# Kernel tuning notes

Hardware: AMD Instinct MI355X
Metric: run time of the kernel (lower is better)

The kernel has to match this reference:

```python
import jax, jax.numpy as jnp
import numpy as np

EPS = 1e-5

def layer_norm(x, g, b):
    mu = jnp.mean(x, axis=-1, keepdims=True)
    var = jnp.var(x, axis=-1, keepdims=True)
    return (x - mu) * jax.lax.rsqrt(var + EPS) * g + b

def setup_inputs() -> dict:
    key = jax.random.key(0)
    ks = jax.random.split(key, 8)
    B, N, C, H = 4, 1024, 1024, 16
    Dh = C * 4
    std = 0.02
    return {
        "x": jax.random.normal(ks[0], (B, N, C), dtype=jnp.float32),
        "qkv_w": jax.random.normal(ks[1], (3 * C, C), dtype=jnp.float32) * std,
        "proj_w": jax.random.normal(ks[2], (C, C), dtype=jnp.float32) * std,
        "proj_b": jnp.zeros((C,), dtype=jnp.float32),
        "fc1_w": jax.random.normal(ks[3], (Dh, C), dtype=jnp.float32) * std,
        "fc1_b": jnp.zeros((Dh,), dtype=jnp.float32),
        "fc2_w": jax.random.normal(ks[4], (C, Dh), dtype=jnp.float32) * std,
        "fc2_b": jnp.zeros((C,), dtype=jnp.float32),
        "ln1_g": jnp.ones((C,), dtype=jnp.float32),
        "ln1_b": jnp.zeros((C,), dtype=jnp.float32),
        "ln2_g": jnp.ones((C,), dtype=jnp.float32),
        "ln2_b": jnp.zeros((C,), dtype=jnp.float32),
        "lnh_g": jnp.ones((Dh,), dtype=jnp.float32),
        "lnh_b": jnp.zeros((Dh,), dtype=jnp.float32),
    }

def reference(x, qkv_w, proj_w, proj_b, fc1_w, fc1_b, fc2_w, fc2_b,
              ln1_g, ln1_b, ln2_g, ln2_b, lnh_g, lnh_b):
    B, N, C = x.shape
    H = 16
    Dh = C // H
    scale = Dh ** (-0.5)

    # --- attention sublayer (pre-norm) ---
    h = layer_norm(x, ln1_g, ln1_b)
    qkv = (h @ qkv_w.T).reshape(B, N, 3, H, Dh).transpose(2, 0, 3, 1, 4)  # [3,B,H,N,Dh]
    q, k, v = qkv[0], qkv[1], qkv[2]
    attn = jnp.einsum('bhid,bhjd->bhij', q, k) * scale
    attn = jax.nn.softmax(attn, axis=-1)
    o = jnp.einsum('bhij,bhjd->bhid', attn, v)          # [B,H,N,Dh]
    o = o.transpose(0, 2, 1, 3).reshape(B, N, C)
    o = o @ proj_w.T + proj_b
    x = x + o

    # --- MLP sublayer (pre-norm, with LN on hidden per use_ln=True) ---
    h = layer_norm(x, ln2_g, ln2_b)
    u = jax.nn.gelu(h @ fc1_w.T + fc1_b, approximate=False)  # torch nn.GELU = erf form
    u = layer_norm(u, lnh_g, lnh_b)
    m = u @ fc2_w.T + fc2_b
    return x + m
```

## Files before the change

### kernel.cpp

```cpp
#include <hip/hip_runtime.h>
#include <hip/hip_bf16.h>
#include <math.h>


#define TOKENS 4096
#define CDIM   1024
#define HEADS  16
#define DHEAD  64
#define HID    4096

typedef __attribute__((ext_vector_type(4))) float  floatx4;
typedef __attribute__((ext_vector_type(8))) short  short8;

__global__ __launch_bounds__(256) void cvt_all(
    const float* __restrict__ s0, const float* __restrict__ s1,
    const float* __restrict__ s2, const float* __restrict__ s3,
    __hip_bfloat16* __restrict__ dst)
{
    long i = (long)blockIdx.x * 256 + threadIdx.x;
    const float* src;
    long base;
    if (i < 768l * 1024)       { src = s0; base = 0; }
    else if (i < 1792l * 1024) { src = s1; base = 768l * 1024; }
    else if (i < 2816l * 1024) { src = s2; base = 1792l * 1024; }
    else                       { src = s3; base = 2816l * 1024; }
    float4 v = ((const float4*)src)[i - base];
    __hip_bfloat16 t[4];
    t[0] = __float2bfloat16(v.x);
    t[1] = __float2bfloat16(v.y);
    t[2] = __float2bfloat16(v.z);
    t[3] = __float2bfloat16(v.w);
    *(uint2*)(dst + 4l * i) = *(uint2*)t;
}

__global__ __launch_bounds__(256) void ln_f32_kernel(
    const float* __restrict__ x, const float* __restrict__ g,
    const float* __restrict__ b, __hip_bfloat16* __restrict__ y, int C)
{
    int row = blockIdx.x;
    const float4* xr = (const float4*)(x + (long)row * C);
    uint2* yr = (uint2*)(y + (long)row * C);
    const int C4 = C >> 2;

    float s = 0.f, ss = 0.f;
    for (int i = threadIdx.x; i < C4; i += 256) {
        float4 v = xr[i];
        s  += v.x + v.y + v.z + v.w;
        ss += v.x * v.x + v.y * v.y + v.z * v.z + v.w * v.w;
    }
    #pragma unroll
    for (int d = 32; d; d >>= 1) {
        s  += __shfl_down(s, d);
        ss += __shfl_down(ss, d);
    }
    __shared__ float buf[4][2];
    int wid = threadIdx.x >> 6, lane = threadIdx.x & 63;
    if (lane == 0) { buf[wid][0] = s; buf[wid][1] = ss; }
    __syncthreads();
    if (threadIdx.x == 0) {
        s = buf[0][0] + buf[1][0] + buf[2][0] + buf[3][0];
        ss = buf[0][1] + buf[1][1] + buf[2][1] + buf[3][1];
        buf[0][0] = s; buf[0][1] = ss;
    }
    __syncthreads();
    s = buf[0][0]; ss = buf[0][1];

    float invC = 1.f / (float)C;
    float mu = s * invC;
    float var = ss * invC - mu * mu;
    float inv = rsqrtf(var + 1e-5f);
    const float4* gg = (const float4*)g;
    const float4* bb = (const float4*)b;
    for (int i = threadIdx.x; i < C4; i += 256) {
        float4 v = xr[i], gv = gg[i], bv = bb[i];
        __hip_bfloat16 t[4];
        t[0] = __float2bfloat16((v.x - mu) * inv * gv.x + bv.x);
        t[1] = __float2bfloat16((v.y - mu) * inv * gv.y + bv.y);
        t[2] = __float2bfloat16((v.z - mu) * inv * gv.z + bv.z);
        t[3] = __float2bfloat16((v.w - mu) * inv * gv.w + bv.w);
        yr[i] = *(uint2*)t;
    }
}

__global__ __launch_bounds__(256) void ln_bf16_kernel(
    const __hip_bfloat16* __restrict__ x, const float* __restrict__ g,
    const float* __restrict__ b, __hip_bfloat16* __restrict__ y, int C)
{
    int row = blockIdx.x;
    const uint4* xr = (const uint4*)(x + (long)row * C);
    uint4* yr = (uint4*)(y + (long)row * C);
    const int C8 = C >> 3;

    float s = 0.f, ss = 0.f;
    for (int i = threadIdx.x; i < C8; i += 256) {
        uint4 raw = xr[i];
        const __hip_bfloat16* p = (const __hip_bfloat16*)&raw;
        #pragma unroll
        for (int j = 0; j < 8; ++j) {
            float v = __bfloat162float(p[j]);
            s += v; ss += v * v;
        }
    }
    #pragma unroll
    for (int d = 32; d; d >>= 1) {
        s  += __shfl_down(s, d);
        ss += __shfl_down(ss, d);
    }
    __shared__ float buf[4][2];
    int wid = threadIdx.x >> 6, lane = threadIdx.x & 63;
    if (lane == 0) { buf[wid][0] = s; buf[wid][1] = ss; }
    __syncthreads();
    if (threadIdx.x == 0) {
        s = buf[0][0] + buf[1][0] + buf[2][0] + buf[3][0];
        ss = buf[0][1] + buf[1][1] + buf[2][1] + buf[3][1];
        buf[0][0] = s; buf[0][1] = ss;
    }
    __syncthreads();
    s = buf[0][0]; ss = buf[0][1];

    float invC = 1.f / (float)C;
    float mu = s * invC;
    float var = ss * invC - mu * mu;
    float inv = rsqrtf(var + 1e-5f);
    const float4* gg = (const float4*)g;
    const float4* bb = (const float4*)b;
    for (int i = threadIdx.x; i < C8; i += 256) {
        uint4 raw = xr[i];
        const __hip_bfloat16* p = (const __hip_bfloat16*)&raw;
        float4 g0 = gg[2 * i], g1 = gg[2 * i + 1];
        float4 b0 = bb[2 * i], b1 = bb[2 * i + 1];
        __hip_bfloat16 t[8];
        t[0] = __float2bfloat16((__bfloat162float(p[0]) - mu) * inv * g0.x + b0.x);
        t[1] = __float2bfloat16((__bfloat162float(p[1]) - mu) * inv * g0.y + b0.y);
        t[2] = __float2bfloat16((__bfloat162float(p[2]) - mu) * inv * g0.z + b0.z);
        t[3] = __float2bfloat16((__bfloat162float(p[3]) - mu) * inv * g0.w + b0.w);
        t[4] = __float2bfloat16((__bfloat162float(p[4]) - mu) * inv * g1.x + b1.x);
        t[5] = __float2bfloat16((__bfloat162float(p[5]) - mu) * inv * g1.y + b1.y);
        t[6] = __float2bfloat16((__bfloat162float(p[6]) - mu) * inv * g1.z + b1.z);
        t[7] = __float2bfloat16((__bfloat162float(p[7]) - mu) * inv * g1.w + b1.w);
        yr[i] = *(uint4*)t;
    }
}

#define STR128 80
__global__ __launch_bounds__(256, 3) void gemm128(
    const __hip_bfloat16* __restrict__ A,
    const __hip_bfloat16* __restrict__ W,
    const float* __restrict__ bias,
    __hip_bfloat16* __restrict__ Cout, int M, int N, int K, int act)
{
    __shared__ __align__(16) char Asl[2][128 * STR128];
    __shared__ __align__(16) char Bsl[2][128 * STR128];

    int tid = threadIdx.x;
    int wave = tid >> 6, lane = tid & 63;

    int mt, nt;
    {
        int gx = gridDim.x, gy = gridDim.y;
        int lin = blockIdx.y * gx + blockIdx.x;
        int chunk = gy >> 3;
        int xcd = lin & 7, q = lin >> 3;
        mt = xcd * chunk + (q % chunk);
        nt = q / chunk;
    }
    int bm = mt * 128, bn = nt * 128;
    int wm = wave & 1, wn = wave >> 1;
    int fm = lane & 15, quad = lane >> 4;

    int srow = lane >> 2;
    int skb  = (lane & 3) * 16;

    const __hip_bfloat16* Ap = A + (long)(bm + wave * 16 + srow) * K + (lane & 3) * 8;
    const __hip_bfloat16* Bp = W + (long)(bn + wave * 16 + srow) * K + (lane & 3) * 8;
    const long a64 = (long)64 * K;

    const int nk = K / 32;
    floatx4 acc[4][4] = {};
    const int aoff = (wave * 16 + srow) * STR128 + skb;

    uint4 a0 = *(const uint4*)(Ap);
    uint4 a1 = *(const uint4*)(Ap + a64);
    uint4 b0 = *(const uint4*)(Bp);
    uint4 b1 = *(const uint4*)(Bp + a64);

    *(uint4*)(Asl[0] + aoff) = a0;
    *(uint4*)(Asl[0] + aoff + 64 * STR128) = a1;
    *(uint4*)(Bsl[0] + aoff) = b0;
    *(uint4*)(Bsl[0] + aoff + 64 * STR128) = b1;

    a0 = *(const uint4*)(Ap + 32);
    a1 = *(const uint4*)(Ap + a64 + 32);
    b0 = *(const uint4*)(Bp + 32);
    b1 = *(const uint4*)(Bp + a64 + 32);

    __syncthreads();

    for (int kt = 0; kt < nk; ++kt) {
        const int buf = kt & 1;
        const char* Ab = Asl[buf];
        const char* Bb = Bsl[buf];

        short8 bfr[4];
        #pragma unroll
        for (int j = 0; j < 4; ++j)
            bfr[j] = *(const short8*)(Bb + (wn * 64 + j * 16 + fm) * STR128 + quad * 16);
        #pragma unroll
        for (int i = 0; i < 4; ++i) {
            short8 af = *(const short8*)(Ab + (wm * 64 + i * 16 + fm) * STR128 + quad * 16);
            #pragma unroll
            for (int j = 0; j < 4; ++j)
                acc[i][j] = __builtin_amdgcn_mfma_f32_16x16x32_bf16(
                    af, bfr[j], acc[i][j], 0, 0, 0);
        }

        if (kt + 1 < nk) {
            const int nb = buf ^ 1;
            *(uint4*)(Asl[nb] + aoff) = a0;
            *(uint4*)(Asl[nb] + aoff + 64 * STR128) = a1;
            *(uint4*)(Bsl[nb] + aoff) = b0;
            *(uint4*)(Bsl[nb] + aoff + 64 * STR128) = b1;
            if (kt + 2 < nk) {
                const long o = (long)(kt + 2) * 32;
                a0 = *(const uint4*)(Ap + o);
                a1 = *(const uint4*)(Ap + a64 + o);
                b0 = *(const uint4*)(Bp + o);
                b1 = *(const uint4*)(Bp + a64 + o);
            }
        }
        __syncthreads();
    }

    int mbase = bm + wm * 64;
    int nbase = bn + wn * 64;
    #pragma unroll
    for (int i = 0; i < 4; ++i) {
        #pragma unroll
        for (int j = 0; j < 4; ++j) {
            int ncol = nbase + j * 16 + fm;
            #pragma unroll
            for (int r = 0; r < 4; ++r) {
                int mrow = mbase + i * 16 + quad * 4 + r;
                float v = acc[i][j][r];
                if (bias) v += bias[ncol];
                if (act == 1) {
                    float z = v * (1.5957691216f + 0.0713548162f * v * v);
                    v = v / (1.f + __expf(-z));
                }
                Cout[(long)mrow * N + ncol] = __float2bfloat16(v);
            }
        }
    }
}

__global__ __launch_bounds__(256, 3) void gemm128res(
    const __hip_bfloat16* __restrict__ A,
    const __hip_bfloat16* __restrict__ W,
    const float* __restrict__ bias, const float* __restrict__ residual,
    float* __restrict__ Cout, int M, int N, int K)
{
    __shared__ __align__(16) char Asl[2][128 * STR128];
    __shared__ __align__(16) char Bsl[2][128 * STR128];

    int tid = threadIdx.x;
    int wave = tid >> 6, lane = tid & 63;

    int mt, nt;
    {
        int gx = gridDim.x, gy = gridDim.y;
        int lin = blockIdx.y * gx + blockIdx.x;
        int chunk = gy >> 3;
        int xcd = lin & 7, q = lin >> 3;
        mt = xcd * chunk + (q % chunk);
        nt = q / chunk;
    }
    int bm = mt * 128, bn = nt * 128;
    int wm = wave & 1, wn = wave >> 1;
    int fm = lane & 15, quad = lane >> 4;

    int srow = lane >> 2;
    int skb  = (lane & 3) * 16;

    const __hip_bfloat16* Ap = A + (long)(bm + wave * 16 + srow) * K + (lane & 3) * 8;
    const __hip_bfloat16* Bp = W + (long)(bn + wave * 16 + srow) * K + (lane & 3) * 8;
    const long a64 = (long)64 * K;

    const int nk = K / 32;
    floatx4 acc[4][4] = {};
    const int aoff = (wave * 16 + srow) * STR128 + skb;

    uint4 a0 = *(const uint4*)(Ap);
    uint4 a1 = *(const uint4*)(Ap + a64);
    uint4 b0 = *(const uint4*)(Bp);
    uint4 b1 = *(const uint4*)(Bp + a64);

    *(uint4*)(Asl[0] + aoff) = a0;
    *(uint4*)(Asl[0] + aoff + 64 * STR128) = a1;
    *(uint4*)(Bsl[0] + aoff) = b0;
    *(uint4*)(Bsl[0] + aoff + 64 * STR128) = b1;

    a0 = *(const uint4*)(Ap + 32);
    a1 = *(const uint4*)(Ap + a64 + 32);
    b0 = *(const uint4*)(Bp + 32);
    b1 = *(const uint4*)(Bp + a64 + 32);

    __syncthreads();

    for (int kt = 0; kt < nk; ++kt) {
        const int buf = kt & 1;
        const char* Ab = Asl[buf];
        const char* Bb = Bsl[buf];

        short8 bfr[4];
        #pragma unroll
        for (int j = 0; j < 4; ++j)
            bfr[j] = *(const short8*)(Bb + (wn * 64 + j * 16 + fm) * STR128 + quad * 16);
        #pragma unroll
        for (int i = 0; i < 4; ++i) {
            short8 af = *(const short8*)(Ab + (wm * 64 + i * 16 + fm) * STR128 + quad * 16);
            #pragma unroll
            for (int j = 0; j < 4; ++j)
                acc[i][j] = __builtin_amdgcn_mfma_f32_16x16x32_bf16(
                    af, bfr[j], acc[i][j], 0, 0, 0);
        }

        if (kt + 1 < nk) {
            const int nb = buf ^ 1;
            *(uint4*)(Asl[nb] + aoff) = a0;
            *(uint4*)(Asl[nb] + aoff + 64 * STR128) = a1;
            *(uint4*)(Bsl[nb] + aoff) = b0;
            *(uint4*)(Bsl[nb] + aoff + 64 * STR128) = b1;
            if (kt + 2 < nk) {
                const long o = (long)(kt + 2) * 32;
                a0 = *(const uint4*)(Ap + o);
                a1 = *(const uint4*)(Ap + a64 + o);
                b0 = *(const uint4*)(Bp + o);
                b1 = *(const uint4*)(Bp + a64 + o);
            }
        }
        __syncthreads();
    }

    int mbase = bm + wm * 64;
    int nbase = bn + wn * 64;
    #pragma unroll
    for (int i = 0; i < 4; ++i) {
        #pragma unroll
        for (int j = 0; j < 4; ++j) {
            int ncol = nbase + j * 16 + fm;
            float bv = bias[ncol];
            #pragma unroll
            for (int r = 0; r < 4; ++r) {
                int mrow = mbase + i * 16 + quad * 4 + r;
                long idx = (long)mrow * N + ncol;
                Cout[idx] = acc[i][j][r] + bv + residual[idx];
            }
        }
    }
}

__global__ __launch_bounds__(256) void attn_mfma(
    const __hip_bfloat16* __restrict__ qkv, __hip_bfloat16* __restrict__ o_out)
{
    __shared__ __align__(16) char Ks[2][64 * 144];
    __shared__ __align__(16) char Vt[2][64 * 144];
    __shared__ __align__(16) char Ps[4 * 16 * 144];

    const int C3 = 3 * CDIM;
    int lin = blockIdx.x;
    int xcd = lin & 7, q = lin >> 3;
    int bh = xcd * 8 + (q >> 4);
    int qt = q & 15;
    int b = bh >> 4, hh = bh & 15;
    int tid = threadIdx.x, wave = tid >> 6, lane = tid & 63;
    int l = lane & 15, quad = lane >> 4;

    const __hip_bfloat16* qrow =
        qkv + (long)(b * 1024 + qt * 64 + wave * 16 + l) * C3 + hh * DHEAD;
    short8 qf0 = *(const short8*)(qrow + quad * 8);
    short8 qf1 = *(const short8*)(qrow + 32 + quad * 8);

    char* Psw = Ps + wave * (16 * 144);

    int sc = tid & 7;
    int skl = tid >> 3;

    const __hip_bfloat16* Kbase = qkv + (long)(b * 1024) * C3 + CDIM + hh * DHEAD;
    const __hip_bfloat16* Vbase = qkv + (long)(b * 1024) * C3 + 2 * CDIM + hh * DHEAD;
    const int kpp = skl ^ (sc << 2);

    floatx4 facc[4] = {};
    float mrun = -1e30f, lrun = 0.f;

    uint4 kA0, kA1, vA0, vA1;
    uint4 kB0, kB1, vB0, vB1;

#define GKV(t, k0, k1, v0, v1) { \
    const __hip_bfloat16* Kg = Kbase + (long)((t) * 64) * C3; \
    const __hip_bfloat16* Vg = Vbase + (long)((t) * 64) * C3; \
    k0 = *(const uint4*)(Kg + (long)skl * C3 + sc * 8); \
    k1 = *(const uint4*)(Kg + (long)(skl + 32) * C3 + sc * 8); \
    v0 = *(const uint4*)(Vg + (long)(2 * skl) * C3 + sc * 8); \
    v1 = *(const uint4*)(Vg + (long)(2 * skl + 1) * C3 + sc * 8); }
#define WKV(bf, k0, k1, v0, v1) { \
    *(uint4*)(Ks[bf] + skl * 144 + sc * 16) = k0; \
    *(uint4*)(Ks[bf] + (skl + 32) * 144 + sc * 16) = k1; \
    const ushort* e0 = (const ushort*)&v0; \
    const ushort* e1 = (const ushort*)&v1; \
    _Pragma("unroll") \
    for (int j = 0; j < 8; ++j) { \
        unsigned dw = (unsigned)e0[j] | ((unsigned)e1[j] << 16); \
        *(unsigned*)(Vt[bf] + (sc * 8 + j) * 144 + kpp * 4) = dw; \
    } }

    auto compute = [&](int buf) {
        floatx4 st[4] = {};
        #pragma unroll
        for (int kb = 0; kb < 4; ++kb) {
            short8 k0 = *(const short8*)(Ks[buf] + (kb * 16 + l) * 144 + quad * 16);
            short8 k1 = *(const short8*)(Ks[buf] + (kb * 16 + l) * 144 + 64 + quad * 16);
            st[kb] = __builtin_amdgcn_mfma_f32_16x16x32_bf16(k0, qf0, st[kb], 0, 0, 0);
            st[kb] = __builtin_amdgcn_mfma_f32_16x16x32_bf16(k1, qf1, st[kb], 0, 0, 0);
        }
        float p[16];
        float tm = -1e30f;
        #pragma unroll
        for (int kb = 0; kb < 4; ++kb)
            #pragma unroll
            for (int r = 0; r < 4; ++r) {
                float s = st[kb][r] * 0.125f;
                p[kb * 4 + r] = s;
                tm = fmaxf(tm, s);
            }
        tm = fmaxf(tm, __shfl_xor(tm, 16));
        tm = fmaxf(tm, __shfl_xor(tm, 32));
        float mn = fmaxf(mrun, tm);
        float alpha = __expf(mrun - mn);
        float psum = 0.f;
        #pragma unroll
        for (int i = 0; i < 16; ++i) { p[i] = __expf(p[i] - mn); psum += p[i]; }
        psum += __shfl_xor(psum, 16);
        psum += __shfl_xor(psum, 32);
        lrun = lrun * alpha + psum;
        mrun = mn;

        #pragma unroll
        for (int kb = 0; kb < 4; ++kb) {
            __hip_bfloat16 t[4];
            #pragma unroll
            for (int r = 0; r < 4; ++r) t[r] = __float2bfloat16(p[kb * 4 + r]);
            *(uint2*)(Psw + l * 144 + kb * 32 + quad * 8) = *(const uint2*)t;
        }

        float a0 = __shfl(alpha, quad * 4 + 0);
        float a1 = __shfl(alpha, quad * 4 + 1);
        float a2 = __shfl(alpha, quad * 4 + 2);
        float a3 = __shfl(alpha, quad * 4 + 3);
        #pragma unroll
        for (int db = 0; db < 4; ++db) {
            facc[db][0] *= a0; facc[db][1] *= a1;
            facc[db][2] *= a2; facc[db][3] *= a3;
        }

        short8 pf0 = *(const short8*)(Psw + l * 144 + quad * 16);
        short8 pf1 = *(const short8*)(Psw + l * 144 + 64 + quad * 16);
        #pragma unroll
        for (int db = 0; db < 4; ++db) {
            int d = db * 16 + l;
            int o3 = (d >> 3) & 7;
            short8 v0 = *(const short8*)(Vt[buf] + d * 144 + ((quad ^ o3) << 4));
            short8 v1 = *(const short8*)(Vt[buf] + d * 144 + (((4 + quad) ^ o3) << 4));
            facc[db] = __builtin_amdgcn_mfma_f32_16x16x32_bf16(pf0, v0, facc[db], 0, 0, 0);
            facc[db] = __builtin_amdgcn_mfma_f32_16x16x32_bf16(pf1, v1, facc[db], 0, 0, 0);
        }
    };

    GKV(0, kA0, kA1, vA0, vA1);
    #pragma unroll 1
    for (int kt = 0; kt < 16; kt += 2) {
        WKV(0, kA0, kA1, vA0, vA1);
        __syncthreads();
        GKV(kt + 1, kB0, kB1, vB0, vB1);
        compute(0);
        WKV(1, kB0, kB1, vB0, vB1);
        __syncthreads();
        if (kt + 2 < 16) GKV(kt + 2, kA0, kA1, vA0, vA1);
        compute(1);
    }
#undef GKV
#undef WKV

    float il0 = 1.f / __shfl(lrun, quad * 4 + 0);
    float il1 = 1.f / __shfl(lrun, quad * 4 + 1);
    float il2 = 1.f / __shfl(lrun, quad * 4 + 2);
    float il3 = 1.f / __shfl(lrun, quad * 4 + 3);
    __hip_bfloat16* orow =
        o_out + (long)(b * 1024 + qt * 64 + wave * 16) * CDIM + hh * DHEAD;
    #pragma unroll
    for (int db = 0; db < 4; ++db) {
        int col = db * 16 + l;
        orow[(quad * 4 + 0) * CDIM + col] = __float2bfloat16(facc[db][0] * il0);
        orow[(quad * 4 + 1) * CDIM + col] = __float2bfloat16(facc[db][1] * il1);
        orow[(quad * 4 + 2) * CDIM + col] = __float2bfloat16(facc[db][2] * il2);
        orow[(quad * 4 + 3) * CDIM + col] = __float2bfloat16(facc[db][3] * il3);
    }
}

extern "C" void kernel_launch(void* const* d_in, const int* in_sizes, int n_in,
                              void* d_out, int out_size, void* d_ws, size_t ws_size,
                              hipStream_t stream)
{
    const float* x      = (const float*)d_in[0];
    const float* qkv_w  = (const float*)d_in[1];
    const float* proj_w = (const float*)d_in[2];
    const float* proj_b = (const float*)d_in[3];
    const float* fc1_w  = (const float*)d_in[4];
    const float* fc1_b  = (const float*)d_in[5];
    const float* fc2_w  = (const float*)d_in[6];
    const float* fc2_b  = (const float*)d_in[7];
    const float* ln1_g  = (const float*)d_in[8];
    const float* ln1_b  = (const float*)d_in[9];
    const float* ln2_g  = (const float*)d_in[10];
    const float* ln2_b  = (const float*)d_in[11];
    const float* lnh_g  = (const float*)d_in[12];
    const float* lnh_b  = (const float*)d_in[13];

    float* out = (float*)d_out;

    __hip_bfloat16* wsb     = (__hip_bfloat16*)d_ws;
    __hip_bfloat16* qkvw_bf = wsb;
    __hip_bfloat16* fc1w_bf = qkvw_bf + 3l * 1024 * 1024;
    __hip_bfloat16* fc2w_bf = fc1w_bf + 4l * 1024 * 1024;
    __hip_bfloat16* projw_bf= fc2w_bf + 4l * 1024 * 1024;
    __hip_bfloat16* h_bf    = projw_bf + 1l * 1024 * 1024;
    __hip_bfloat16* qkv_bf  = h_bf + 4l * 1024 * 1024;
    __hip_bfloat16* o_bf    = qkv_bf + 12l * 1024 * 1024;
    __hip_bfloat16* u_bf    = o_bf + 4l * 1024 * 1024;

    cvt_all<<<12288, 256, 0, stream>>>(qkv_w, fc1_w, fc2_w, proj_w, qkvw_bf);

    ln_f32_kernel<<<TOKENS, 256, 0, stream>>>(x, ln1_g, ln1_b, h_bf, CDIM);
    gemm128<<<dim3(3072 / 128, TOKENS / 128), 256, 0, stream>>>(
        h_bf, qkvw_bf, nullptr, qkv_bf, TOKENS, 3072, CDIM, 0);
    attn_mfma<<<1024, 256, 0, stream>>>(qkv_bf, o_bf);
    gemm128res<<<dim3(CDIM / 128, TOKENS / 128), 256, 0, stream>>>(
        o_bf, projw_bf, proj_b, x, out, TOKENS, CDIM, CDIM);
    ln_f32_kernel<<<TOKENS, 256, 0, stream>>>(out, ln2_g, ln2_b, h_bf, CDIM);
    gemm128<<<dim3(HID / 128, TOKENS / 128), 256, 0, stream>>>(
        h_bf, fc1w_bf, fc1_b, u_bf, TOKENS, HID, CDIM, 1);
    ln_bf16_kernel<<<TOKENS, 256, 0, stream>>>(u_bf, lnh_g, lnh_b, u_bf, HID);
    gemm128res<<<dim3(CDIM / 128, TOKENS / 128), 256, 0, stream>>>(
        u_bf, fc2w_bf, fc2_b, out, out, TOKENS, CDIM, HID);
}
```

Before: 370.0 us.

## Use direct global-to-LDS loads in GEMM and split-K atomics for fc2

Replaces the register-staged, double-buffered GEMM with a kernel that issues global_load_lds directly into unpadded LDS tiles with a 64-wide K step. The fc2 GEMM is split along K into four slices whose partial results are atomically added into the output, which already holds the residual. This aims to cut register staging and VGPR traffic and to raise parallelism for the narrow fc2 GEMM. In exchange it loses load/compute overlap from double buffering, may hit LDS bank conflicts without padding, and adds fp32 atomic traffic and nondeterministic summation order.

```diff
diff --git a/kernel.cpp b/kernel.cpp
--- a/kernel.cpp
+++ b/kernel.cpp
@@ -11,6 +11,14 @@
 
 typedef __attribute__((ext_vector_type(4))) float  floatx4;
 typedef __attribute__((ext_vector_type(8))) short  short8;
+
+__device__ __forceinline__ void gl_lds16(const void* g, void* l)
+{
+    __builtin_amdgcn_global_load_lds(
+        (const __attribute__((address_space(1))) unsigned int*)g,
+        (__attribute__((address_space(3))) unsigned int*)l,
+        16, 0, 0);
+}
 
 __global__ __launch_bounds__(256) void cvt_all(
     const float* __restrict__ s0, const float* __restrict__ s1,
@@ -142,15 +150,14 @@
     }
 }
 
-#define STR128 80
-__global__ __launch_bounds__(256, 3) void gemm128(
+__global__ __launch_bounds__(256, 3) void gemm_gl(
     const __hip_bfloat16* __restrict__ A,
     const __hip_bfloat16* __restrict__ W,
     const float* __restrict__ bias,
-    __hip_bfloat16* __restrict__ Cout, int M, int N, int K, int act)
-{
-    __shared__ __align__(16) char Asl[2][128 * STR128];
-    __shared__ __align__(16) char Bsl[2][128 * STR128];
+    void* __restrict__ Cout, int M, int N, int K, int mode)
+{
+    __shared__ __align__(16) __hip_bfloat16 Asl[128][64];
+    __shared__ __align__(16) __hip_bfloat16 Bsl[128][64];
 
     int tid = threadIdx.x;
     int wave = tid >> 6, lane = tid & 63;
@@ -168,64 +175,51 @@
     int wm = wave & 1, wn = wave >> 1;
     int fm = lane & 15, quad = lane >> 4;
 
-    int srow = lane >> 2;
-    int skb  = (lane & 3) * 16;
-
-    const __hip_bfloat16* Ap = A + (long)(bm + wave * 16 + srow) * K + (lane & 3) * 8;
-    const __hip_bfloat16* Bp = W + (long)(bn + wave * 16 + srow) * K + (lane & 3) * 8;
-    const long a64 = (long)64 * K;
-
-    const int nk = K / 32;
+    const int KS = K / gridDim.z;
+    const long kz = (long)blockIdx.z * KS;
+    const int nk = KS / 64;
+
+    const int rsub = lane >> 3;
+    const int csub = lane & 7;
+    const __hip_bfloat16* gA[4];
+    const __hip_bfloat16* gB[4];
+    char* dA[4];
+    char* dB[4];
+    #pragma unroll
+    for (int j = 0; j < 4; ++j) {
+        int seg = wave * 4 + j;
+        gA[j] = A + (long)(bm + seg * 8 + rsub) * K + kz + csub * 8;
+        gB[j] = W + (long)(bn + seg * 8 + rsub) * K + kz + csub * 8;
+        dA[j] = (char*)&Asl[0][0] + seg * 1024;
+        dB[j] = (char*)&Bsl[0][0] + seg * 1024;
+    }
+
     floatx4 acc[4][4] = {};
-    const int aoff = (wave * 16 + srow) * STR128 + skb;
-
-    uint4 a0 = *(const uint4*)(Ap);
-    uint4 a1 = *(const uint4*)(Ap + a64);
-    uint4 b0 = *(const uint4*)(Bp);
-    uint4 b1 = *(const uint4*)(Bp + a64);
-
-    *(uint4*)(Asl[0] + aoff) = a0;
-    *(uint4*)(Asl[0] + aoff + 64 * STR128) = a1;
-    *(uint4*)(Bsl[0] + aoff) = b0;
-    *(uint4*)(Bsl[0] + aoff + 64 * STR128) = b1;
-
-    a0 = *(const uint4*)(Ap + 32);
-    a1 = *(const uint4*)(Ap + a64 + 32);
-    b0 = *(const uint4*)(Bp + 32);
-    b1 = *(const uint4*)(Bp + a64 + 32);
-
-    __syncthreads();
 
     for (int kt = 0; kt < nk; ++kt) {
-        const int buf = kt & 1;
-        const char* Ab = Asl[buf];
-        const char* Bb = Bsl[buf];
-
-        short8 bfr[4];
-        #pragma unroll
-        for (int j = 0; j < 4; ++j)
-            bfr[j] = *(const short8*)(Bb + (wn * 64 + j * 16 + fm) * STR128 + quad * 16);
-        #pragma unroll
-        for (int i = 0; i < 4; ++i) {
-            short8 af = *(const short8*)(Ab + (wm * 64 + i * 16 + fm) * STR128 + quad * 16);
+        const long ko = (long)kt * 64;
+        #pragma unroll
+        for (int j = 0; j < 4; ++j) {
+            gl_lds16(gA[j] + ko, dA[j]);
+            gl_lds16(gB[j] + ko, dB[j]);
+        }
+        __syncthreads();
+
+        #pragma unroll
+        for (int kh = 0; kh < 2; ++kh) {
+            short8 bq[4];
             #pragma unroll
             for (int j = 0; j < 4; ++j)
-                acc[i][j] = __builtin_amdgcn_mfma_f32_16x16x32_bf16(
-                    af, bfr[j], acc[i][j], 0, 0, 0);
-        }
-
-        if (kt + 1 < nk) {
-            const int nb = buf ^ 1;
-            *(uint4*)(Asl[nb] + aoff) = a0;
-            *(uint4*)(Asl[nb] + aoff + 64 * STR128) = a1;
-            *(uint4*)(Bsl[nb] + aoff) = b0;
-            *(uint4*)(Bsl[nb] + aoff + 64 * STR128) = b1;
-            if (kt + 2 < nk) {
-                const long o = (long)(kt + 2) * 32;
-                a0 = *(const uint4*)(Ap + o);
-                a1 = *(const uint4*)(Ap + a64 + o);
-                b0 = *(const uint4*)(Bp + o);
-                b1 = *(const uint4*)(Bp + a64 + o);
+                bq[j] = *(const short8*)((const char*)&Bsl[0][0]
+                        + (wn * 64 + j * 16 + fm) * 128 + kh * 64 + quad * 16);
+            #pragma unroll
+            for (int i = 0; i < 4; ++i) {
+                short8 af = *(const short8*)((const char*)&Asl[0][0]
+                        + (wm * 64 + i * 16 + fm) * 128 + kh * 64 + quad * 16);
+                #pragma unroll
+                for (int j = 0; j < 4; ++j)
+                    acc[i][j] = __builtin_amdgcn_mfma_f32_16x16x32_bf16(
+                        af, bq[j], acc[i][j], 0, 0, 0);
             }
         }
         __syncthreads();
@@ -233,26 +227,46 @@
 
     int mbase = bm + wm * 64;
     int nbase = bn + wn * 64;
-    #pragma unroll
-    for (int i = 0; i < 4; ++i) {
-        #pragma unroll
-        for (int j = 0; j < 4; ++j) {
-            int ncol = nbase + j * 16 + fm;
-            #pragma unroll
-            for (int r = 0; r < 4; ++r) {
-                int mrow = mbase + i * 16 + quad * 4 + r;
-                float v = acc[i][j][r];
-                if (bias) v += bias[ncol];
-                if (act == 1) {
-                    float z = v * (1.5957691216f + 0.0713548162f * v * v);
-                    v = v / (1.f + __expf(-z));
+    if (mode == 2) {
+        float* Cf = (float*)Cout;
+        const bool addb = (blockIdx.z == 0);
+        #pragma unroll
+        for (int i = 0; i < 4; ++i) {
+            #pragma unroll
+            for (int j = 0; j < 4; ++j) {
+                int ncol = nbase + j * 16 + fm;
+                float bv = addb ? bias[ncol] : 0.f;
+                #pragma unroll
+                for (int r = 0; r < 4; ++r) {
+                    int mrow = mbase + i * 16 + quad * 4 + r;
+                    atomicAdd(&Cf[(long)mrow * N + ncol], acc[i][j][r] + bv);
                 }
-                Cout[(long)mrow * N + ncol] = __float2bfloat16(v);
             }
         }
-    }
-}
-
+    } else {
+        __hip_bfloat16* Cb = (__hip_bfloat16*)Cout;
+        #pragma unroll
+        for (int i = 0; i < 4; ++i) {
+            #pragma unroll
+            for (int j = 0; j < 4; ++j) {
+                int ncol = nbase + j * 16 + fm;
+                #pragma unroll
+                for (int r = 0; r < 4; ++r) {
+                    int mrow = mbase + i * 16 + quad * 4 + r;
+                    float v = acc[i][j][r];
+                    if (bias) v += bias[ncol];
+                    if (mode == 1) {
+                        float z = v * (1.5957691216f + 0.0713548162f * v * v);
+                        v = v / (1.f + __expf(-z));
+                    }
+                    Cb[(long)mrow * N + ncol] = __float2bfloat16(v);
+                }
+            }
+        }
+    }
+}
+
+#define STR128 80
 __global__ __launch_bounds__(256, 3) void gemm128res(
     const __hip_bfloat16* __restrict__ A,
     const __hip_bfloat16* __restrict__ W,
@@ -540,15 +554,15 @@
     cvt_all<<<12288, 256, 0, stream>>>(qkv_w, fc1_w, fc2_w, proj_w, qkvw_bf);
 
     ln_f32_kernel<<<TOKENS, 256, 0, stream>>>(x, ln1_g, ln1_b, h_bf, CDIM);
-    gemm128<<<dim3(3072 / 128, TOKENS / 128), 256, 0, stream>>>(
+    gemm_gl<<<dim3(3072 / 128, TOKENS / 128, 1), 256, 0, stream>>>(
         h_bf, qkvw_bf, nullptr, qkv_bf, TOKENS, 3072, CDIM, 0);
     attn_mfma<<<1024, 256, 0, stream>>>(qkv_bf, o_bf);
     gemm128res<<<dim3(CDIM / 128, TOKENS / 128), 256, 0, stream>>>(
         o_bf, projw_bf, proj_b, x, out, TOKENS, CDIM, CDIM);
     ln_f32_kernel<<<TOKENS, 256, 0, stream>>>(out, ln2_g, ln2_b, h_bf, CDIM);
-    gemm128<<<dim3(HID / 128, TOKENS / 128), 256, 0, stream>>>(
+    gemm_gl<<<dim3(HID / 128, TOKENS / 128, 1), 256, 0, stream>>>(
         h_bf, fc1w_bf, fc1_b, u_bf, TOKENS, HID, CDIM, 1);
     ln_bf16_kernel<<<TOKENS, 256, 0, stream>>>(u_bf, lnh_g, lnh_b, u_bf, HID);
-    gemm128res<<<dim3(CDIM / 128, TOKENS / 128), 256, 0, stream>>>(
-        u_bf, fc2w_bf, fc2_b, out, out, TOKENS, CDIM, HID);
-}
+    gemm_gl<<<dim3(CDIM / 128, TOKENS / 128, 4), 256, 0, stream>>>(
+        u_bf, fc2w_bf, fc2_b, out, TOKENS, CDIM, HID, 2);
+}
```

New measurement: 381.7 us. 1.03x slower.
